# Kernel tuning notes

Hardware: AMD Instinct MI355X
Metric: run time of the kernel (lower is better)

## Reference

```python
import jax, jax.numpy as jnp
import numpy as np

NUM_ITERATIONS = 3


def _squash(s):
    # Faithful to the torch code: squash over dim=2 of s_j [B,1,nu,us,1],
    # which is the num_units axis. In our [B, nu, us] layout that is axis=1.
    mag_sq = jnp.sum(s ** 2, axis=1, keepdims=True)  # [B,1,us]
    mag = jnp.sqrt(mag_sq)
    return mag_sq / (1.0 + mag_sq) * (s / mag)


def setup_inputs() -> dict:
    key = jax.random.key(0)
    k1, k2 = jax.random.split(key)
    B, in_units, in_channels, num_units, unit_size = 256, 8, 1152, 10, 16
    x = jax.random.normal(k1, (B, in_units, in_channels), dtype=jnp.float32)
    W = jax.random.normal(k2, (1, in_channels, num_units, unit_size, in_units), dtype=jnp.float32)
    return {"x": x, "W": W}


def reference(x, W):
    B = x.shape[0]
    W0 = W[0]  # [ic, nu, us, iu]
    ic, nu = W0.shape[0], W0.shape[1]
    xt = jnp.swapaxes(x, 1, 2)  # [B, ic, iu]
    # u_hat = W @ x per (batch, in_channel, out_unit): [B, ic, nu, us]
    u_hat = jnp.einsum('cdui,bci->bcdu', W0, xt)
    b_ij = jnp.zeros((ic, nu), dtype=x.dtype)
    v = None
    for _ in range(NUM_ITERATIONS):
        c_ij = jax.nn.softmax(b_ij, axis=0)              # softmax over in_channels
        s_j = jnp.einsum('cd,bcdu->bdu', c_ij, u_hat)    # [B, nu, us]
        v = _squash(s_j)                                 # [B, nu, us]
        # agreement: <u_hat, v> over unit_size, mean over batch -> [ic, nu]
        agree = jnp.einsum('bcdu,bdu->cd', u_hat, v) / B
        b_ij = b_ij + agree
    return v  # [B, num_units, unit_size]
```

## Files before the change

### kernel.cpp

```cpp
#include <hip/hip_runtime.h>
#include <math.h>

#define B_  256
#define IU  8
#define IC  1152
#define NU  10
#define US  16
#define CCH 9
#define NCH 128
#define BT  64
#define NBLK 512
#define XSP 516
#define SPSTRIDE ((size_t)NCH * B_ * NU * US)

__device__ __forceinline__ float gld(const float* p) {
    return __hip_atomic_load(p, __ATOMIC_RELAXED, __HIP_MEMORY_SCOPE_AGENT);
}
__device__ __forceinline__ void gst(float* p, float v) {
    __hip_atomic_store(p, v, __ATOMIC_RELAXED, __HIP_MEMORY_SCOPE_AGENT);
}
__device__ __forceinline__ unsigned uld(const unsigned* p) {
    return __hip_atomic_load(p, __ATOMIC_RELAXED, __HIP_MEMORY_SCOPE_AGENT);
}
__device__ __forceinline__ void ust(unsigned* p, unsigned v) {
    __hip_atomic_store(p, v, __ATOMIC_RELAXED, __HIP_MEMORY_SCOPE_AGENT);
}

__device__ __forceinline__ void gridbar(unsigned* bar) {
    __syncthreads();
    if (threadIdx.x == 0) {
        const int bid = blockIdx.x;
        const int leaf = bid >> 3;
        const int mid  = bid >> 6;
        unsigned* myR1 = bar + (96 + leaf) * 32;
        unsigned g = uld(myR1);
        unsigned a = __hip_atomic_fetch_add(bar + leaf * 32, 1u,
                                            __ATOMIC_RELAXED, __HIP_MEMORY_SCOPE_AGENT);
        if (a == 7u) {
            ust(bar + leaf * 32, 0u);
            unsigned b2 = __hip_atomic_fetch_add(bar + (64 + mid) * 32, 1u,
                                                 __ATOMIC_RELAXED, __HIP_MEMORY_SCOPE_AGENT);
            if (b2 == 7u) {
                ust(bar + (64 + mid) * 32, 0u);
                unsigned c2 = __hip_atomic_fetch_add(bar + 72 * 32, 1u,
                                                     __ATOMIC_RELAXED, __HIP_MEMORY_SCOPE_AGENT);
                if (c2 == 7u) {
                    ust(bar + 72 * 32, 0u);
#pragma unroll
                    for (int k = 0; k < 8; k++)
                        ust(bar + (80 + k) * 32, g + 1u);
                }
                while (uld(bar + (80 + mid) * 32) == g)
                    __builtin_amdgcn_s_sleep(8);
#pragma unroll
                for (int j = 0; j < 8; j++)
                    ust(bar + (96 + mid * 8 + j) * 32, g + 1u);
            }
        }
        while (uld(myR1) == g)
            __builtin_amdgcn_s_sleep(16);
    }
    __syncthreads();
}

__global__ __launch_bounds__(256, 2) void mega(const float* __restrict__ x,
                                               const float* __restrict__ W,
                                               float* __restrict__ sp,
                                               float* __restrict__ vb0,
                                               float* __restrict__ vb1,
                                               float* __restrict__ bij,
                                               float* __restrict__ esum,
                                               unsigned* __restrict__ ticket,
                                               float* __restrict__ out,
                                               unsigned* __restrict__ bar) {
    __shared__ float4 ws[CCH * NU * 2 * 16];
    __shared__ __align__(16) float xs[CCH * XSP];
    __shared__ float aux[NU * US];
    __shared__ float cs[NU * CCH];
    __shared__ int lastflag;

    const int tid = threadIdx.x;
    const int bid = blockIdx.x;
    const int grp = bid & 7;
    const int slot_ = bid >> 3;
    const int ch = ((slot_ >> 2) << 3) | grp;
    const int bt = slot_ & 3;
    const int b0 = bt * BT, c0 = ch * CCH;

    const float4* wg = (const float4*)W + (size_t)c0 * 320;
    for (int q = tid; q < CCH * NU * 32; q += 256) {
        int h = q & 1, u = (q >> 1) & 15, cd = q >> 5;
        ws[(cd * 2 + h) * 16 + u] = wg[q];
    }
    for (int idx = tid; idx < CCH * BT * IU; idx += 256) {
        int cc = idx % CCH;
        int r = idx / CCH;
        xs[cc * XSP + r] = x[((size_t)(b0 + (r >> 3)) * IU + (r & 7)) * IC + c0 + cc];
    }

    const int uq = tid & 15;
    const int bs = tid >> 4;

    for (int iter = 0; iter < 3; ++iter) {
        float* spb = sp + (size_t)iter * SPSTRIDE;

        __syncthreads();
        if (iter == 0) {
            for (int q = tid; q < NU * CCH; q += 256) cs[q] = 1.0f;
        } else {
            for (int q = tid; q < NU * CCH; q += 256) {
                int d = q / CCH, cc = q - d * CCH;
                float es = gld(esum + (iter - 1) * 16 + d);
                cs[q] = expf(gld(bij + (size_t)d * IC + c0 + cc)) / es;
            }
        }
        __syncthreads();
        const float scale = iter ? 1.0f : (1.0f / (float)IC);

        {
            float acc[4][NU];
#pragma unroll
            for (int bb = 0; bb < 4; bb++)
#pragma unroll
                for (int d = 0; d < NU; d++) acc[bb][d] = 0.0f;

#pragma unroll 3
            for (int cc = 0; cc < CCH; cc++) {
                float4 xv0[4], xv1[4];
#pragma unroll
                for (int bb = 0; bb < 4; bb++) {
                    const float4* xp = (const float4*)(xs + cc * XSP + (bs + 16 * bb) * IU);
                    xv0[bb] = xp[0]; xv1[bb] = xp[1];
                }
#pragma unroll
                for (int d = 0; d < NU; d++) {
                    float4 w0 = ws[((cc * NU + d) * 2 + 0) * 16 + uq];
                    float4 w1 = ws[((cc * NU + d) * 2 + 1) * 16 + uq];
                    const float cw = cs[d * CCH + cc];
#pragma unroll
                    for (int bb = 0; bb < 4; bb++) {
                        float uh = w0.x * xv0[bb].x + w0.y * xv0[bb].y + w0.z * xv0[bb].z + w0.w * xv0[bb].w
                                 + w1.x * xv1[bb].x + w1.y * xv1[bb].y + w1.z * xv1[bb].z + w1.w * xv1[bb].w;
                        acc[bb][d] = fmaf(cw, uh, acc[bb][d]);
                    }
                }
            }
#pragma unroll
            for (int bb = 0; bb < 4; bb++) {
                const int b = b0 + bs + 16 * bb;
#pragma unroll
                for (int d = 0; d < NU; d++)
                    gst(spb + (((size_t)ch * B_ + b) * NU + d) * US + uq, acc[bb][d] * scale);
            }
        }
        gridbar(bar);

        if (bid < B_) {
            if (tid < 160) {
                const int part = tid & 3;
                const int sl = tid >> 2;
                const float4* s4p = (const float4*)spb;
                float4 a = make_float4(0.f, 0.f, 0.f, 0.f);
#pragma unroll 8
                for (int k = 0; k < 32; ++k) {
                    float4 t = s4p[((size_t)(part * 32 + k) * B_ + bid) * 40 + sl];
                    a.x += t.x; a.y += t.y; a.z += t.z; a.w += t.w;
                }
                a.x += __shfl_xor(a.x, 1, 64); a.y += __shfl_xor(a.y, 1, 64);
                a.z += __shfl_xor(a.z, 1, 64); a.w += __shfl_xor(a.w, 1, 64);
                a.x += __shfl_xor(a.x, 2, 64); a.y += __shfl_xor(a.y, 2, 64);
                a.z += __shfl_xor(a.z, 2, 64); a.w += __shfl_xor(a.w, 2, 64);
                if (part == 0) {
                    aux[sl * 4 + 0] = a.x; aux[sl * 4 + 1] = a.y;
                    aux[sl * 4 + 2] = a.z; aux[sl * 4 + 3] = a.w;
                }
            }
            __syncthreads();
            if (tid < NU * US) {
                float s = aux[tid];
                float msq = 0.0f;
#pragma unroll
                for (int dd = 0; dd < NU; dd++) {
                    float t = aux[dd * US + uq];
                    msq = fmaf(t, t, msq);
                }
                float f = msq / ((1.0f + msq) * sqrtf(msq));
                if (iter == 2)
                    out[(size_t)bid * (NU * US) + tid] = s * f;
                else {
                    float* vdst = (iter == 0) ? vb0 : vb1;
                    gst(vdst + (size_t)bid * (NU * US) + tid, s * f);
                }
            }
        }
        if (iter == 2) return;
        gridbar(bar);

        {
            const int cl = tid >> 4;
            const float* vb = (iter == 0) ? vb0 : vb1;
            if (cl < CCH) {
                float4 wA[NU], wB[NU];
#pragma unroll
                for (int d = 0; d < NU; d++) {
                    wA[d] = ws[((cl * NU + d) * 2 + 0) * 16 + uq];
                    wB[d] = ws[((cl * NU + d) * 2 + 1) * 16 + uq];
                }
                float accd[NU];
#pragma unroll
                for (int d = 0; d < NU; d++) accd[d] = 0.0f;
                const int bstag = (cl & 3) * 7;
#pragma unroll 4
                for (int blx = 0; blx < BT; blx++) {
                    const int bl = (blx + bstag) & 63;
                    const float* xp = xs + cl * XSP + bl * IU;
                    float4 x0 = *(const float4*)xp;
                    float4 x1 = *(const float4*)(xp + 4);
                    const float* vp = vb + (size_t)(b0 + bl) * (NU * US) + uq;
#pragma unroll
                    for (int d = 0; d < NU; d++) {
                        float uh = wA[d].x * x0.x + wA[d].y * x0.y + wA[d].z * x0.z + wA[d].w * x0.w
                                 + wB[d].x * x1.x + wB[d].y * x1.y + wB[d].z * x1.z + wB[d].w * x1.w;
                        accd[d] = fmaf(uh, vp[d * US], accd[d]);
                    }
                }
#pragma unroll
                for (int d = 0; d < NU; d++) {
                    float a = accd[d];
                    a += __shfl_xor(a, 1, 64);
                    a += __shfl_xor(a, 2, 64);
                    a += __shfl_xor(a, 4, 64);
                    a += __shfl_xor(a, 8, 64);
                    if (uq == 0)
                        atomicAdd(bij + (size_t)d * IC + c0 + cl, a * (1.0f / (float)B_));
                }
            }
            __syncthreads();
            if (tid == 0) {
                unsigned old = __hip_atomic_fetch_add(ticket + iter * 128 + ch, 1u,
                                                      __ATOMIC_RELAXED,
                                                      __HIP_MEMORY_SCOPE_AGENT);
                lastflag = (old == 3u);
            }
            __syncthreads();
            if (lastflag && tid < NU) {
                float es = 0.0f;
#pragma unroll
                for (int cc = 0; cc < CCH; cc++)
                    es += expf(gld(bij + (size_t)tid * IC + c0 + cc));
                atomicAdd(esum + iter * 16 + tid, es);
            }
        }
        gridbar(bar);
    }
}

extern "C" void kernel_launch(void* const* d_in, const int* in_sizes, int n_in,
                              void* d_out, int out_size, void* d_ws, size_t ws_size,
                              hipStream_t stream) {
    (void)in_sizes; (void)n_in; (void)out_size; (void)ws_size;
    const float* x = (const float*)d_in[0];
    const float* W = (const float*)d_in[1];
    float* out = (float*)d_out;

    unsigned* bar = (unsigned*)d_ws;
    unsigned* ticket = bar + 5120;
    float* esum = (float*)(ticket + 256);
    float* bij = esum + 32;
    float* sp  = bij + (size_t)NU * IC;
    float* vb0 = sp + 3 * SPSTRIDE;
    float* vb1 = vb0 + (size_t)B_ * NU * US;

    hipMemsetAsync(d_ws, 0, (5120 + 256) * 4 + 32 * 4 + (size_t)NU * IC * 4, stream);
    mega<<<NBLK, 256, 0, stream>>>(x, W, sp, vb0, vb1, bij, esum, ticket, out, bar);
}
```

Before: 189.3 us.

## Reduce s_j via global atomics and fuse squash into agreement pass

Each block now adds its partial s_j into one shared per-iteration buffer with atomicAdd, replacing the per-chunk partial buffer and its separate reduction pass. Every block that needs v recomputes the squash on the fly while it computes agreement, so one grid barrier and the v buffer write per iteration are gone. The cost is heavy float atomic contention (128 chunks adding into each element), redundant squash work in every block, a larger memset of the accumulation buffers, and run-to-run nondeterministic summation order.

```diff
diff --git a/kernel.cpp b/kernel.cpp
--- a/kernel.cpp
+++ b/kernel.cpp
@@ -11,13 +11,10 @@
 #define BT  64
 #define NBLK 512
 #define XSP 516
-#define SPSTRIDE ((size_t)NCH * B_ * NU * US)
+#define SBSTRIDE ((size_t)B_ * NU * US)
 
 __device__ __forceinline__ float gld(const float* p) {
     return __hip_atomic_load(p, __ATOMIC_RELAXED, __HIP_MEMORY_SCOPE_AGENT);
-}
-__device__ __forceinline__ void gst(float* p, float v) {
-    __hip_atomic_store(p, v, __ATOMIC_RELAXED, __HIP_MEMORY_SCOPE_AGENT);
 }
 __device__ __forceinline__ unsigned uld(const unsigned* p) {
     return __hip_atomic_load(p, __ATOMIC_RELAXED, __HIP_MEMORY_SCOPE_AGENT);
@@ -65,9 +62,7 @@
 
 __global__ __launch_bounds__(256, 2) void mega(const float* __restrict__ x,
                                                const float* __restrict__ W,
-                                               float* __restrict__ sp,
-                                               float* __restrict__ vb0,
-                                               float* __restrict__ vb1,
+                                               float* __restrict__ sb,
                                                float* __restrict__ bij,
                                                float* __restrict__ esum,
                                                unsigned* __restrict__ ticket,
@@ -102,7 +97,7 @@
     const int bs = tid >> 4;
 
     for (int iter = 0; iter < 3; ++iter) {
-        float* spb = sp + (size_t)iter * SPSTRIDE;
+        float* sbb = sb + (size_t)iter * SBSTRIDE;
 
         __syncthreads();
         if (iter == 0) {
@@ -148,57 +143,35 @@
 #pragma unroll
             for (int bb = 0; bb < 4; bb++) {
                 const int b = b0 + bs + 16 * bb;
+                float* rowp = sbb + (size_t)b * (NU * US) + uq;
 #pragma unroll
                 for (int d = 0; d < NU; d++)
-                    gst(spb + (((size_t)ch * B_ + b) * NU + d) * US + uq, acc[bb][d] * scale);
+                    atomicAdd(rowp + d * US, acc[bb][d] * scale);
             }
         }
         gridbar(bar);
 
-        if (bid < B_) {
-            if (tid < 160) {
-                const int part = tid & 3;
-                const int sl = tid >> 2;
-                const float4* s4p = (const float4*)spb;
-                float4 a = make_float4(0.f, 0.f, 0.f, 0.f);
-#pragma unroll 8
-                for (int k = 0; k < 32; ++k) {
-                    float4 t = s4p[((size_t)(part * 32 + k) * B_ + bid) * 40 + sl];
-                    a.x += t.x; a.y += t.y; a.z += t.z; a.w += t.w;
-                }
-                a.x += __shfl_xor(a.x, 1, 64); a.y += __shfl_xor(a.y, 1, 64);
-                a.z += __shfl_xor(a.z, 1, 64); a.w += __shfl_xor(a.w, 1, 64);
-                a.x += __shfl_xor(a.x, 2, 64); a.y += __shfl_xor(a.y, 2, 64);
-                a.z += __shfl_xor(a.z, 2, 64); a.w += __shfl_xor(a.w, 2, 64);
-                if (part == 0) {
-                    aux[sl * 4 + 0] = a.x; aux[sl * 4 + 1] = a.y;
-                    aux[sl * 4 + 2] = a.z; aux[sl * 4 + 3] = a.w;
-                }
-            }
-            __syncthreads();
-            if (tid < NU * US) {
-                float s = aux[tid];
-                float msq = 0.0f;
-#pragma unroll
-                for (int dd = 0; dd < NU; dd++) {
-                    float t = aux[dd * US + uq];
-                    msq = fmaf(t, t, msq);
-                }
-                float f = msq / ((1.0f + msq) * sqrtf(msq));
-                if (iter == 2)
+        if (iter == 2) {
+            if (bid < B_) {
+                if (tid < NU * US) aux[tid] = sbb[(size_t)bid * (NU * US) + tid];
+                __syncthreads();
+                if (tid < NU * US) {
+                    float s = aux[tid];
+                    float msq = 0.0f;
+#pragma unroll
+                    for (int dd = 0; dd < NU; dd++) {
+                        float t = aux[dd * US + uq];
+                        msq = fmaf(t, t, msq);
+                    }
+                    float f = msq / ((1.0f + msq) * sqrtf(msq));
                     out[(size_t)bid * (NU * US) + tid] = s * f;
-                else {
-                    float* vdst = (iter == 0) ? vb0 : vb1;
-                    gst(vdst + (size_t)bid * (NU * US) + tid, s * f);
-                }
-            }
-        }
-        if (iter == 2) return;
-        gridbar(bar);
+                }
+            }
+            return;
+        }
 
         {
             const int cl = tid >> 4;
-            const float* vb = (iter == 0) ? vb0 : vb1;
             if (cl < CCH) {
                 float4 wA[NU], wB[NU];
 #pragma unroll
@@ -213,15 +186,23 @@
 #pragma unroll 4
                 for (int blx = 0; blx < BT; blx++) {
                     const int bl = (blx + bstag) & 63;
+                    const float* sp_ = sbb + (size_t)(b0 + bl) * (NU * US) + uq;
+                    float sv[NU];
+#pragma unroll
+                    for (int d = 0; d < NU; d++) sv[d] = sp_[d * US];
+                    float msq = 0.0f;
+#pragma unroll
+                    for (int d = 0; d < NU; d++) msq = fmaf(sv[d], sv[d], msq);
+                    const float f = msq / ((1.0f + msq) * sqrtf(msq));
+
                     const float* xp = xs + cl * XSP + bl * IU;
                     float4 x0 = *(const float4*)xp;
                     float4 x1 = *(const float4*)(xp + 4);
-                    const float* vp = vb + (size_t)(b0 + bl) * (NU * US) + uq;
 #pragma unroll
                     for (int d = 0; d < NU; d++) {
                         float uh = wA[d].x * x0.x + wA[d].y * x0.y + wA[d].z * x0.z + wA[d].w * x0.w
                                  + wB[d].x * x1.x + wB[d].y * x1.y + wB[d].z * x1.z + wB[d].w * x1.w;
-                        accd[d] = fmaf(uh, vp[d * US], accd[d]);
+                        accd[d] = fmaf(uh, sv[d] * f, accd[d]);
                     }
                 }
 #pragma unroll
@@ -267,10 +248,10 @@
     unsigned* ticket = bar + 5120;
     float* esum = (float*)(ticket + 256);
     float* bij = esum + 32;
-    float* sp  = bij + (size_t)NU * IC;
-    float* vb0 = sp + 3 * SPSTRIDE;
-    float* vb1 = vb0 + (size_t)B_ * NU * US;
-
-    hipMemsetAsync(d_ws, 0, (5120 + 256) * 4 + 32 * 4 + (size_t)NU * IC * 4, stream);
-    mega<<<NBLK, 256, 0, stream>>>(x, W, sp, vb0, vb1, bij, esum, ticket, out, bar);
-}
+    float* sb  = bij + (size_t)NU * IC;
+
+    size_t zbytes = (5120 + 256) * 4 + 32 * 4 + (size_t)NU * IC * 4
+                  + 3 * SBSTRIDE * 4;
+    hipMemsetAsync(d_ws, 0, zbytes, stream);
+    mega<<<NBLK, 256, 0, stream>>>(x, W, sb, bij, esum, ticket, out, bar);
+}
```

Result: slower. 233.4 us (+23.3%).
